# Kernel tuning notes

Measured on AMD Instinct MI355X. Metric: run time of the kernel, lower is better.

## Reference

```python
import jax, jax.numpy as jnp
import numpy as np

BATCH = 8
IMG = 224
PATCH = 16
IN_CH = 8
D_MODEL = 768
DEPTH = 4
D_INNER = 2 * D_MODEL          # 1536
D_STATE = 16
DT_RANK = D_MODEL // 16        # 48
D_CONV = 4
NUM_CLASSES = 1000
EPS = 1e-5


def setup_inputs() -> dict:
    key = jax.random.key(0)
    ks = jax.random.split(key, 16)
    g = lambda i, shape, s=0.02: jax.random.normal(ks[i], shape, jnp.float32) * s
    L = DEPTH
    inp = {}
    inp['x'] = jax.random.normal(ks[0], (BATCH, IN_CH, IMG, IMG), jnp.float32)
    # patch embed: Conv3d(1, D, (1,p,p)) == shared 2D conv applied to every channel
    inp['patch_w'] = g(1, (D_MODEL, PATCH, PATCH))
    inp['patch_b'] = jnp.zeros((D_MODEL,), jnp.float32)
    inp['channel_embed'] = g(2, (IN_CH, D_MODEL))
    # per-block params (stacked over depth)
    inp['norm_w'] = jnp.ones((L, D_MODEL), jnp.float32)
    inp['norm_b'] = jnp.zeros((L, D_MODEL), jnp.float32)
    inp['in_proj_w'] = g(3, (L, 2 * D_INNER, D_MODEL))
    inp['conv_w'] = g(4, (L, D_INNER, D_CONV), 0.1)
    inp['conv_b'] = jnp.zeros((L, D_INNER), jnp.float32)
    inp['x_proj_w'] = g(5, (L, DT_RANK + 2 * D_STATE, D_INNER))
    inp['dt_proj_w'] = g(6, (L, D_INNER, DT_RANK), 0.1)
    inp['dt_proj_b'] = jnp.full((L, D_INNER), -4.6, jnp.float32)  # softplus^-1(0.01)
    inp['A_log'] = jnp.tile(jnp.log(jnp.arange(1, D_STATE + 1, dtype=jnp.float32)), (L, D_INNER, 1))
    inp['D_param'] = jnp.ones((L, D_INNER), jnp.float32)
    inp['ssm_norm_w'] = jnp.ones((L, D_INNER), jnp.float32)
    inp['ssm_norm_b'] = jnp.zeros((L, D_INNER), jnp.float32)
    inp['out_proj_w'] = g(7, (L, D_MODEL, D_INNER), 0.02 / np.sqrt(L))
    # final norm + classification head
    inp['norm_f_w'] = jnp.ones((D_MODEL,), jnp.float32)
    inp['norm_f_b'] = jnp.zeros((D_MODEL,), jnp.float32)
    inp['head_w'] = g(8, (NUM_CLASSES, D_MODEL))
    inp['head_b'] = jnp.zeros((NUM_CLASSES,), jnp.float32)
    return inp


def _ln(x, w, b):
    mu = x.mean(-1, keepdims=True)
    var = ((x - mu) ** 2).mean(-1, keepdims=True)
    return (x - mu) * jax.lax.rsqrt(var + EPS) * w + b


def _silu(x):
    return x * jax.nn.sigmoid(x)


def _mamba(h, ipw, cw, cb, xpw, dtw, dtb, Alog, Dp, snw, snb, opw):
    # h: [B, L, D_MODEL]
    B, Lseq, _ = h.shape
    xz = jnp.einsum('bld,ed->ble', h, ipw)               # [B, L, 2*di]
    x, z = jnp.split(xz, 2, axis=-1)
    # causal depthwise conv1d along L (kernel D_CONV)
    xp = jnp.pad(x, ((0, 0), (D_CONV - 1, 0), (0, 0)))
    xc = cb + sum(xp[:, k:k + Lseq, :] * cw[:, k] for k in range(D_CONV))
    x = _silu(xc)
    dbc = jnp.einsum('bld,ed->ble', x, xpw)              # [B, L, dt_rank+2N]
    dt_r = dbc[..., :DT_RANK]
    Bm = dbc[..., DT_RANK:DT_RANK + D_STATE]
    Cm = dbc[..., DT_RANK + D_STATE:]
    dt = jax.nn.softplus(jnp.einsum('blr,dr->bld', dt_r, dtw) + dtb)  # [B, L, di]
    A = -jnp.exp(Alog)                                    # [di, N]

    def step(hstate, t):
        dt_t, B_t, C_t, x_t = t                           # [B,di],[B,N],[B,N],[B,di]
        dA = jnp.exp(dt_t[..., None] * A)                 # [B, di, N]
        hstate = dA * hstate + (dt_t * x_t)[..., None] * B_t[:, None, :]
        y = jnp.einsum('bdn,bn->bd', hstate, C_t)
        return hstate, y

    h0 = jnp.zeros((B, D_INNER, D_STATE), x.dtype)
    xs = (dt.transpose(1, 0, 2), Bm.transpose(1, 0, 2),
          Cm.transpose(1, 0, 2), x.transpose(1, 0, 2))
    _, ys = jax.lax.scan(step, h0, xs)                    # [L, B, di]
    y = ys.transpose(1, 0, 2) + Dp * x
    y = _ln(y, snw, snb)                                  # norm-after-SSM
    y = y * _silu(z)
    return jnp.einsum('ble,de->bld', y, opw)


def reference(x, patch_w, patch_b, channel_embed, norm_w, norm_b, in_proj_w,
              conv_w, conv_b, x_proj_w, dt_proj_w, dt_proj_b, A_log, D_param,
              ssm_norm_w, ssm_norm_b, out_proj_w, norm_f_w, norm_f_b,
              head_w, head_b):
    B, C, H, W = x.shape
    hg, wg = H // PATCH, W // PATCH
    # shared-filter patch embed per channel: [B,C,hg,wg,D]
    xp = x.reshape(B, C, hg, PATCH, wg, PATCH)
    emb = jnp.einsum('bchpwq,dpq->bchwd', xp, patch_w) + patch_b
    emb = emb + channel_embed[None, :, None, None, :]
    # Channel-First scan order -> token order (h, w, C): [B, hg*wg*C, D]
    tok = emb.transpose(0, 2, 3, 1, 4).reshape(B, hg * wg * C, D_MODEL)

    hidden, residual = tok, None
    for i in range(DEPTH):
        residual = hidden if residual is None else residual + hidden
        hn = _ln(residual, norm_w[i], norm_b[i])
        hidden = _mamba(hn, in_proj_w[i], conv_w[i], conv_b[i], x_proj_w[i],
                        dt_proj_w[i], dt_proj_b[i], A_log[i], D_param[i],
                        ssm_norm_w[i], ssm_norm_b[i], out_proj_w[i])
    residual = residual + hidden
    hf = _ln(residual, norm_f_w, norm_f_b)
    pooled = hf.mean(axis=1)                              # mean pooling head
    return pooled @ head_w.T + head_b
```

## Files before the change

### kernel.cpp

```cpp
#include <hip/hip_runtime.h>
#include <hip/hip_bf16.h>

typedef __hip_bfloat16 bf16;
typedef __attribute__((ext_vector_type(8))) short short8;
typedef __attribute__((ext_vector_type(4))) float float4v;

#define BATCH 8
#define SEQ   1568
#define M_TOK (BATCH*SEQ)
#define DM    768
#define DI    1536
#define DS    16
#define DTR   48
#define NCLS  1000
#define LAYERS 4
#define CHUNK 112
#define NCH   14

__device__ __forceinline__ float b2f(bf16 v){ return __bfloat162float(v); }
__device__ __forceinline__ bf16  f2b(float v){ return __float2bfloat16(v); }
__device__ __forceinline__ float us2f(unsigned short u){
    unsigned v = ((unsigned)u) << 16; float f; __builtin_memcpy(&f, &v, 4); return f;
}
__device__ __forceinline__ void gload_lds16(const void* g, void* l){
    __builtin_amdgcn_global_load_lds(
        (const __attribute__((address_space(1))) void*)g,
        (__attribute__((address_space(3))) void*)l, 16, 0, 0);
}
template<int CTRL>
__device__ __forceinline__ float dpp_add(float p){
    int pi; __builtin_memcpy(&pi, &p, 4);
    int mi = __builtin_amdgcn_update_dpp(pi, pi, CTRL, 0xF, 0xF, false);
    float m; __builtin_memcpy(&m, &mi, 4);
    return p + m;
}

__global__ void detect_dtype(const unsigned short* __restrict__ probe, unsigned* __restrict__ flag)
{
    if (threadIdx.x == 0 && blockIdx.x == 0) flag[0] = (probe[0] == 0) ? 1u : 0u;
}

__global__ __launch_bounds__(256)
void to_bf16(const unsigned* __restrict__ flag, const void* __restrict__ src,
             bf16* __restrict__ dst, int n)
{
    int i = blockIdx.x*256 + threadIdx.x;
    if (i >= n) return;
    dst[i] = flag[0] ? f2b(((const float*)src)[i]) : ((const bf16*)src)[i];
}

__global__ __launch_bounds__(256)
void to_f32(const unsigned* __restrict__ flag, const void* __restrict__ src,
            float* __restrict__ dst, int n)
{
    int i = blockIdx.x*256 + threadIdx.x;
    if (i >= n) return;
    dst[i] = flag[0] ? ((const float*)src)[i] : b2f(((const bf16*)src)[i]);
}

__global__ __launch_bounds__(256)
void gather_patches(const bf16* __restrict__ x, bf16* __restrict__ Ap, int b0)
{
    size_t idx = (size_t)blockIdx.x*256 + threadIdx.x;
    int i = (int)(idx & 255);
    int m = (int)(idx >> 8);
    int b = b0 + m / SEQ, s = m % SEQ;
    int hw = s >> 3, c = s & 7;
    int h = hw / 14, w = hw % 14;
    int p = i >> 4, q = i & 15;
    Ap[idx] = x[(((size_t)(b*8 + c)*224) + h*16 + p)*224 + w*16 + q];
}

__global__ __launch_bounds__(256)
void gemm_mfma(const bf16* __restrict__ A, int lda,
               const bf16* __restrict__ W, int ldw,
               float* __restrict__ Cf, bf16* __restrict__ Cb, int ldc,
               const float* __restrict__ bias, const float* __restrict__ chan,
               int M, int N, int K, int epi)
{
    __shared__ short As[128*40];
    __shared__ short Bs[128*40];
    int tid  = threadIdx.x;
    int m0   = blockIdx.x*128, n0 = blockIdx.y*128;
    int lane = tid & 63, wv = tid >> 6;
    int wm = (wv >> 1)*64, wn = (wv & 1)*64;
    int l15 = lane & 15, quad = lane >> 4;

    float4v acc[4][4];
    #pragma unroll
    for (int i = 0; i < 4; ++i)
        #pragma unroll
        for (int j = 0; j < 4; ++j) acc[i][j] = (float4v){0.f,0.f,0.f,0.f};

    const short8 zv8 = {0,0,0,0,0,0,0,0};
    for (int k0 = 0; k0 < K; k0 += 32) {
        #pragma unroll
        for (int u = 0; u < 2; ++u) {
            int c   = tid*2 + u;
            int row = c >> 2, ch = c & 3;
            bool kok = (k0 + ch*8 + 8) <= K;
            short8 va = (kok && m0 + row < M)
                ? *(const short8*)((const short*)A + (size_t)(m0+row)*lda + k0 + ch*8) : zv8;
            *(short8*)(As + row*40 + ch*8) = va;
            short8 vb = (kok && n0 + row < N)
                ? *(const short8*)((const short*)W + (size_t)(n0+row)*ldw + k0 + ch*8) : zv8;
            *(short8*)(Bs + row*40 + ch*8) = vb;
        }
        __syncthreads();
        short8 av[4], bv[4];
        #pragma unroll
        for (int i = 0; i < 4; ++i) av[i] = *(const short8*)(As + (wm + i*16 + l15)*40 + quad*8);
        #pragma unroll
        for (int j = 0; j < 4; ++j) bv[j] = *(const short8*)(Bs + (wn + j*16 + l15)*40 + quad*8);
        #pragma unroll
        for (int i = 0; i < 4; ++i)
            #pragma unroll
            for (int j = 0; j < 4; ++j)
                acc[i][j] = __builtin_amdgcn_mfma_f32_16x16x32_bf16(av[i], bv[j], acc[i][j], 0, 0, 0);
        __syncthreads();
    }

    #pragma unroll
    for (int i = 0; i < 4; ++i) {
        #pragma unroll
        for (int j = 0; j < 4; ++j) {
            int gn = n0 + wn + j*16 + l15;
            if (gn >= N) continue;
            #pragma unroll
            for (int r = 0; r < 4; ++r) {
                int gm = m0 + wm + i*16 + quad*4 + r;
                if (gm >= M) continue;
                float v = acc[i][j][r];
                size_t off = (size_t)gm*ldc + gn;
                if (epi == 0)      Cb[off] = f2b(v);
                else if (epi == 1) {
                    v += bias[gn];
                    v = (v > 20.f) ? v : log1pf(__expf(v));
                    Cb[off] = f2b(v);
                }
                else if (epi == 2) Cf[off] += v;
                else               Cf[off] = v + bias[gn] + chan[(size_t)(gm & 7)*N + gn];
            }
        }
    }
}

__global__ __launch_bounds__(256)
void gemm_mfma_fast(const bf16* __restrict__ A, int lda,
                    const bf16* __restrict__ W, int ldw,
                    float* __restrict__ Cf, bf16* __restrict__ Cb, int ldc,
                    const float* __restrict__ bias, const float* __restrict__ chan,
                    int N, int K, int epi)
{
    __shared__ short As[128*32];
    __shared__ short Bs[128*32];
    int tid  = threadIdx.x;
    int m0   = blockIdx.x*128, n0 = blockIdx.y*128;
    int lane = tid & 63, wv = tid >> 6;
    int wm = (wv >> 1)*64, wn = (wv & 1)*64;
    int l15 = lane & 15, quad = lane >> 4;

    int srow = (lane >> 2);
    int skof = (lane & 3) * 8;

    float4v acc[4][4];
    #pragma unroll
    for (int i = 0; i < 4; ++i)
        #pragma unroll
        for (int j = 0; j < 4; ++j) acc[i][j] = (float4v){0.f,0.f,0.f,0.f};

    const short* Ab = (const short*)A;
    const short* Wb = (const short*)W;

    for (int k0 = 0; k0 < K; k0 += 32) {
        #pragma unroll
        for (int u = 0; u < 2; ++u) {
            int c = wv*2 + u;
            int row = c*16 + srow;
            gload_lds16(Ab + (size_t)(m0+row)*lda + k0 + skof, As + c*512);
            gload_lds16(Wb + (size_t)(n0+row)*ldw + k0 + skof, Bs + c*512);
        }
        __syncthreads();
        short8 av[4], bv[4];
        #pragma unroll
        for (int i = 0; i < 4; ++i) av[i] = *(const short8*)(As + (wm + i*16 + l15)*32 + quad*8);
        #pragma unroll
        for (int j = 0; j < 4; ++j) bv[j] = *(const short8*)(Bs + (wn + j*16 + l15)*32 + quad*8);
        #pragma unroll
        for (int i = 0; i < 4; ++i)
            #pragma unroll
            for (int j = 0; j < 4; ++j)
                acc[i][j] = __builtin_amdgcn_mfma_f32_16x16x32_bf16(av[i], bv[j], acc[i][j], 0, 0, 0);
        __syncthreads();
    }

    #pragma unroll
    for (int i = 0; i < 4; ++i) {
        #pragma unroll
        for (int j = 0; j < 4; ++j) {
            int gn = n0 + wn + j*16 + l15;
            #pragma unroll
            for (int r = 0; r < 4; ++r) {
                int gm = m0 + wm + i*16 + quad*4 + r;
                float v = acc[i][j][r];
                size_t off = (size_t)gm*ldc + gn;
                if (epi == 0)      Cb[off] = f2b(v);
                else if (epi == 1) {
                    v += bias[gn];
                    v = (v > 20.f) ? v : log1pf(__expf(v));
                    Cb[off] = f2b(v);
                }
                else if (epi == 2) Cf[off] += v;
                else               Cf[off] = v + bias[gn] + chan[(size_t)(gm & 7)*N + gn];
            }
        }
    }
}

__global__ __launch_bounds__(256)
void ln768(const float* __restrict__ X, const float* __restrict__ w,
           const float* __restrict__ bb, bf16* __restrict__ out)
{
    __shared__ float red[8];
    size_t t = blockIdx.x;
    const float* x = X + t*DM;
    float v[3]; float s = 0.f, s2 = 0.f;
    #pragma unroll
    for (int r = 0; r < 3; ++r) {
        v[r] = x[threadIdx.x + 256*r];
        s += v[r]; s2 += v[r]*v[r];
    }
    #pragma unroll
    for (int o = 32; o; o >>= 1) { s += __shfl_down(s, o, 64); s2 += __shfl_down(s2, o, 64); }
    if ((threadIdx.x & 63) == 0) { red[threadIdx.x >> 6] = s; red[(threadIdx.x >> 6) + 4] = s2; }
    __syncthreads();
    s  = red[0]+red[1]+red[2]+red[3];
    s2 = red[4]+red[5]+red[6]+red[7];
    float mu  = s * (1.f/DM);
    float inv = rsqrtf(fmaxf(s2*(1.f/DM) - mu*mu, 0.f) + 1e-5f);
    #pragma unroll
    for (int r = 0; r < 3; ++r) {
        int i = threadIdx.x + 256*r;
        out[t*DM + i] = f2b((v[r]-mu)*inv*w[i] + bb[i]);
    }
}

__global__ __launch_bounds__(256)
void conv_silu(const bf16* __restrict__ xh, const float* __restrict__ cw,
               const float* __restrict__ cb, bf16* __restrict__ xc)
{
    size_t idx = (size_t)blockIdx.x*256 + threadIdx.x;
    int dv = (int)(idx % (DI/8));
    int m  = (int)(idx / (DI/8));
    int b = m / SEQ, t = m % SEQ;
    int d = dv*8;

    float4v cwq[8];
    #pragma unroll
    for (int j = 0; j < 8; ++j) cwq[j] = *(const float4v*)(cw + (size_t)(d+j)*4);

    float acc[8];
    #pragma unroll
    for (int j = 0; j < 8; ++j) acc[j] = cb[d+j];

    #pragma unroll
    for (int k = 0; k < 4; ++k) {
        int tt = t + k - 3;
        if (tt >= 0) {
            short8 v = *(const short8*)((const short*)xh + (size_t)(b*SEQ + tt)*DI + d);
            #pragma unroll
            for (int j = 0; j < 8; ++j)
                acc[j] += us2f((unsigned short)v[j]) * cwq[j][k];
        }
    }
    short8 o;
    #pragma unroll
    for (int j = 0; j < 8; ++j) {
        float sig = 1.f/(1.f + __expf(-acc[j]));
        bf16 r = f2b(acc[j]*sig);
        unsigned short u; __builtin_memcpy(&u, &r, 2); o[j] = (short)u;
    }
    *(short8*)((short*)xc + idx*8) = o;
}


__global__ __launch_bounds__(256)
void scan_pass1(const bf16* __restrict__ dt, const bf16* __restrict__ x,
                const bf16* __restrict__ dbc, const float* __restrict__ Alog,
                float* __restrict__ hend, float* __restrict__ Pprod, int nin2)
{
    __shared__ float dtT[2][64][20], xT[2][64][20];
    __shared__ float BsT[2][16][16];
    int c  = blockIdx.x / nin2;
    int r  = blockIdx.x % nin2;
    int b  = r / 24;
    int d0 = (r % 24) * 64;
    int tid = threadIdx.x;
    int sq = tid & 3;
    int dl = tid >> 2;
    int d  = d0 + dl;

    float4v Aq = *(const float4v*)(Alog + (size_t)d*DS + sq*4);
    float A2[4], h[4];
    #pragma unroll
    for (int k = 0; k < 4; ++k) { A2[k] = -__expf(Aq[k]) * 1.44269504f; h[k] = 0.f; }
    float sdt = 0.f;

    int js = tid >> 4, dg = tid & 15;
    bool doB = tid < 64;
    int j2 = tid >> 2;

    const unsigned short* pdt = (const unsigned short*)dt + ((size_t)b*SEQ + js)*DI + d0 + dg*4;
    const unsigned short* px  = (const unsigned short*)x  + ((size_t)b*SEQ + js)*DI + d0 + dg*4;
    const unsigned short* pbc = (const unsigned short*)dbc + ((size_t)b*SEQ + (j2 & 15))*80 + DTR + sq*4;
    int tbase = c * CHUNK;
    const int NT = CHUNK/16;

    ushort4 vdt, vx, vbc;
    auto stage = [&](int buf){
        dtT[buf][dg*4+0][js] = us2f(vdt.x); dtT[buf][dg*4+1][js] = us2f(vdt.y);
        dtT[buf][dg*4+2][js] = us2f(vdt.z); dtT[buf][dg*4+3][js] = us2f(vdt.w);
        xT [buf][dg*4+0][js] = us2f(vx.x);  xT [buf][dg*4+1][js] = us2f(vx.y);
        xT [buf][dg*4+2][js] = us2f(vx.z);  xT [buf][dg*4+3][js] = us2f(vx.w);
        if (doB)
            *(float4v*)&BsT[buf][j2][sq*4] =
                (float4v){us2f(vbc.x), us2f(vbc.y), us2f(vbc.z), us2f(vbc.w)};
    };
    auto fetch = [&](int T){
        vdt = *(const ushort4*)(pdt + (size_t)(tbase + T*16)*DI);
        vx  = *(const ushort4*)(px  + (size_t)(tbase + T*16)*DI);
        if (doB) vbc = *(const ushort4*)(pbc + (size_t)(tbase + T*16)*80);
    };

    fetch(0); stage(0); fetch(1);
    __syncthreads();

    for (int t = 0; t < NT; ++t) {
        int cur = t & 1;
        if (t+1 < NT) stage(cur^1);
        if (t+2 < NT) fetch(t+2);
        #pragma unroll
        for (int jj = 0; jj < 16; jj += 4) {
            float4v dtq = *(const float4v*)&dtT[cur][dl][jj];
            float4v xq  = *(const float4v*)&xT [cur][dl][jj];
            #pragma unroll
            for (int k2 = 0; k2 < 4; ++k2) {
                float dtv = dtq[k2];
                float dtx = dtv * xq[k2];
                float4v Bq = *(const float4v*)&BsT[cur][jj+k2][sq*4];
                #pragma unroll
                for (int k = 0; k < 4; ++k)
                    h[k] = exp2f(dtv*A2[k])*h[k] + dtx*Bq[k];
                sdt += dtv;
            }
        }
        __syncthreads();
    }
    size_t o = (((size_t)c*nin2 + r)*256 + tid)*4;
    *(float4v*)(hend + o) = (float4v){h[0], h[1], h[2], h[3]};
    *(float4v*)(Pprod + o) = (float4v){exp2f(A2[0]*sdt), exp2f(A2[1]*sdt),
                                       exp2f(A2[2]*sdt), exp2f(A2[3]*sdt)};
}

__global__ __launch_bounds__(256)
void scan_mid(const float* __restrict__ hend, const float* __restrict__ Pprod,
              float* __restrict__ hstart, int nin2)
{
    int r = blockIdx.x, tid = threadIdx.x;
    float4v h = (float4v){0.f,0.f,0.f,0.f};
    *(float4v*)(hstart + ((size_t)r*256 + tid)*4) = h;
    for (int c = 1; c < NCH; ++c) {
        size_t p = (((size_t)(c-1)*nin2 + r)*256 + tid)*4;
        float4v P  = *(const float4v*)(Pprod + p);
        float4v he = *(const float4v*)(hend + p);
        h = P*h + he;
        *(float4v*)(hstart + (((size_t)c*nin2 + r)*256 + tid)*4) = h;
    }
}

__global__ __launch_bounds__(256)
void scan_pass2(const bf16* __restrict__ dt, const bf16* __restrict__ x,
                const bf16* __restrict__ dbc, const float* __restrict__ Alog,
                const float* __restrict__ Dpar, const float* __restrict__ hstart,
                bf16* __restrict__ y, int nin2)
{
    __shared__ float dtT[2][64][20], xT[2][64][20];
    __shared__ float BsT[2][16][16], CsT[2][16][16];
    __shared__ bf16  ys[16][64];
    int c  = blockIdx.x / nin2;
    int r  = blockIdx.x % nin2;
    int b  = r / 24;
    int d0 = (r % 24) * 64;
    int tid = threadIdx.x;
    int sq = tid & 3;
    int dl = tid >> 2;
    int d  = d0 + dl;

    float4v Aq = *(const float4v*)(Alog + (size_t)d*DS + sq*4);
    float A2[4], h[4];
    {
        float4v h0 = *(const float4v*)(hstart + (((size_t)c*nin2 + r)*256 + tid)*4);
        #pragma unroll
        for (int k = 0; k < 4; ++k) { A2[k] = -__expf(Aq[k]) * 1.44269504f; h[k] = h0[k]; }
    }
    float Dv = Dpar[d];

    int js = tid >> 4, dg = tid & 15;
    bool doBC = tid < 128;
    int j2 = (tid & 63) >> 2;

    const unsigned short* pdt = (const unsigned short*)dt + ((size_t)b*SEQ + js)*DI + d0 + dg*4;
    const unsigned short* px  = (const unsigned short*)x  + ((size_t)b*SEQ + js)*DI + d0 + dg*4;
    const unsigned short* pbc = (const unsigned short*)dbc + ((size_t)b*SEQ + j2)*80 + DTR
                                + ((tid >= 64) ? DS : 0) + sq*4;
    float* bc0 = (tid < 64) ? &BsT[0][j2][sq*4] : &CsT[0][j2][sq*4];
    int tbase = c * CHUNK;
    const int NT = CHUNK/16;

    ushort4 vdt, vx, vbc;
    auto stage = [&](int buf){
        dtT[buf][dg*4+0][js] = us2f(vdt.x); dtT[buf][dg*4+1][js] = us2f(vdt.y);
        dtT[buf][dg*4+2][js] = us2f(vdt.z); dtT[buf][dg*4+3][js] = us2f(vdt.w);
        xT [buf][dg*4+0][js] = us2f(vx.x);  xT [buf][dg*4+1][js] = us2f(vx.y);
        xT [buf][dg*4+2][js] = us2f(vx.z);  xT [buf][dg*4+3][js] = us2f(vx.w);
        if (doBC)
            *(float4v*)(bc0 + (size_t)buf*256) =
                (float4v){us2f(vbc.x), us2f(vbc.y), us2f(vbc.z), us2f(vbc.w)};
    };
    auto fetch = [&](int T){
        vdt = *(const ushort4*)(pdt + (size_t)(tbase + T*16)*DI);
        vx  = *(const ushort4*)(px  + (size_t)(tbase + T*16)*DI);
        if (doBC) vbc = *(const ushort4*)(pbc + (size_t)(tbase + T*16)*80);
    };

    fetch(0); stage(0); fetch(1);
    __syncthreads();

    for (int t = 0; t < NT; ++t) {
        int cur = t & 1;
        if (t+1 < NT) stage(cur^1);
        if (t+2 < NT) fetch(t+2);

        #pragma unroll
        for (int jj = 0; jj < 16; jj += 4) {
            float4v dtq = *(const float4v*)&dtT[cur][dl][jj];
            float4v xq  = *(const float4v*)&xT [cur][dl][jj];
            #pragma unroll
            for (int k2 = 0; k2 < 4; ++k2) {
                float dtv = dtq[k2];
                float xv  = xq[k2];
                float dtx = dtv * xv;
                float4v Bq = *(const float4v*)&BsT[cur][jj+k2][sq*4];
                float4v Cq = *(const float4v*)&CsT[cur][jj+k2][sq*4];
                float p = 0.f;
                #pragma unroll
                for (int k = 0; k < 4; ++k) {
                    h[k] = exp2f(dtv*A2[k])*h[k] + dtx*Bq[k];
                    p += h[k]*Cq[k];
                }
                p = dpp_add<0xB1>(p);
                p = dpp_add<0x4E>(p);
                if (sq == 0) ys[jj+k2][dl] = f2b(p + Dv*xv);
            }
        }
        __syncthreads();
        {
            size_t rowm = (size_t)(b*SEQ + tbase + t*16 + js);
            ushort4 vy = *(const ushort4*)((const unsigned short*)&ys[js][0] + dg*4);
            *(ushort4*)((unsigned short*)y + rowm*DI + d0 + dg*4) = vy;
        }
        __syncthreads();
    }
}

__global__ __launch_bounds__(256)
void gate_ln(const bf16* __restrict__ y, const bf16* __restrict__ z,
             const float* __restrict__ w, const float* __restrict__ bb,
             bf16* __restrict__ out)
{
    __shared__ float red[8];
    size_t t = blockIdx.x;
    const bf16* yy = y + t*DI;
    const bf16* zz = z + t*DI;
    float v[6]; float s = 0.f, s2 = 0.f;
    #pragma unroll
    for (int r = 0; r < 6; ++r) {
        v[r] = b2f(yy[threadIdx.x + 256*r]);
        s += v[r]; s2 += v[r]*v[r];
    }
    #pragma unroll
    for (int o = 32; o; o >>= 1) { s += __shfl_down(s, o, 64); s2 += __shfl_down(s2, o, 64); }
    if ((threadIdx.x & 63) == 0) { red[threadIdx.x >> 6] = s; red[(threadIdx.x >> 6) + 4] = s2; }
    __syncthreads();
    s  = red[0]+red[1]+red[2]+red[3];
    s2 = red[4]+red[5]+red[6]+red[7];
    float mu  = s * (1.f/DI);
    float inv = rsqrtf(fmaxf(s2*(1.f/DI) - mu*mu, 0.f) + 1e-5f);
    #pragma unroll
    for (int r = 0; r < 6; ++r) {
        int i = threadIdx.x + 256*r;
        float zv = b2f(zz[i]);
        float sig = 1.f/(1.f + __expf(-zv));
        out[t*DI + i] = f2b(((v[r]-mu)*inv*w[i] + bb[i]) * (zv*sig));
    }
}

__global__ __launch_bounds__(256)
void pool_kernel(const bf16* __restrict__ hf, float* __restrict__ pooled)
{
    int idx = blockIdx.x*256 + threadIdx.x;
    int b = idx / DM, dm = idx % DM;
    const bf16* p = hf + (size_t)b*SEQ*DM + dm;
    float s = 0.f;
    for (int t = 0; t < SEQ; ++t) s += b2f(p[(size_t)t*DM]);
    pooled[idx] = s * (1.f/SEQ);
}

__global__ __launch_bounds__(256)
void head_kernel(const unsigned* __restrict__ flag,
                 const float* __restrict__ pooled, const bf16* __restrict__ hw,
                 const float* __restrict__ hb, void* __restrict__ out)
{
    int idx = blockIdx.x*256 + threadIdx.x;
    if (idx >= BATCH*NCLS) return;
    int b = idx & 7, n = idx >> 3;
    const float* p = pooled + b*DM;
    const unsigned short* w = (const unsigned short*)hw + (size_t)n*DM;
    float acc = hb[n];
    for (int k = 0; k < DM; k += 4) {
        ushort4 wv = *(const ushort4*)(w + k);
        acc += p[k]*us2f(wv.x) + p[k+1]*us2f(wv.y) + p[k+2]*us2f(wv.z) + p[k+3]*us2f(wv.w);
    }
    int o = b*NCLS + n;
    if (flag[0]) ((float*)out)[o] = acc;
    else         ((bf16*)out)[o]  = f2b(acc);
}

extern "C" void kernel_launch(void* const* d_in, const int* in_sizes, int n_in,
                              void* d_out, int out_size, void* d_ws, size_t ws_size,
                              hipStream_t stream)
{
    (void)n_in; (void)out_size;
    dim3 blk(256);

    const bool is_f32[21] = { false, false, true, true, true, true, false, true, true,
                              false, false, true,  true, true, true, true, false,
                              true,  true,  false, true };

    size_t off = 0;
    auto carve = [&](size_t bytes) -> void* {
        void* q = (char*)d_ws + off;
        off += (bytes + 255) & ~(size_t)255;
        return q;
    };

    unsigned* flag = (unsigned*)carve(256);
    void* canon[21];
    for (int i = 0; i < 21; ++i)
        canon[i] = carve((size_t)in_sizes[i] * (is_f32[i] ? 4 : 2));

    float* residual = (float*)carve((size_t)M_TOK*DM*4);
    bf16*  hn       = (bf16*) carve((size_t)M_TOK*DM*2);
    float* pooled   = (float*)carve((size_t)BATCH*DM*4);

    const size_t scanbuf1 = (size_t)NCH*96*256*4;
    const size_t inner1 = 4*(((size_t)SEQ*DI*2 + 255) & ~(size_t)255)
                          + (((size_t)SEQ*80*2 + 255) & ~(size_t)255)
                          + 3*((scanbuf1 + 255) & ~(size_t)255);
    int g = 8;
    while (g > 1 && off + (size_t)g*inner1 > ws_size) g >>= 1;

    bf16* xh  = (bf16*)carve((size_t)g*SEQ*DI*2);
    bf16* zh  = (bf16*)carve((size_t)g*SEQ*DI*2);
    bf16* xc  = (bf16*)carve((size_t)g*SEQ*DI*2);
    bf16* dtb = (bf16*)carve((size_t)g*SEQ*DI*2);
    bf16* dbc = (bf16*)carve((size_t)g*SEQ*80*2);
    float* hend   = (float*)carve((size_t)g*scanbuf1);
    float* Pprod  = (float*)carve((size_t)g*scanbuf1);
    float* hstart = (float*)carve((size_t)g*scanbuf1);
    bf16* Ap    = xh;
    bf16* ybuf  = xh;
    bf16* gated = dtb;

    detect_dtype<<<1, 64, 0, stream>>>((const unsigned short*)d_in[4], flag);
    for (int i = 0; i < 21; ++i) {
        int n = in_sizes[i];
        int gr = (n + 255)/256;
        if (is_f32[i]) to_f32 <<<gr, blk, 0, stream>>>(flag, d_in[i], (float*)canon[i], n);
        else           to_bf16<<<gr, blk, 0, stream>>>(flag, d_in[i], (bf16*) canon[i], n);
    }

    const bf16*  xin   = (const bf16*) canon[0];
    const bf16*  pw    = (const bf16*) canon[1];
    const float* pb    = (const float*)canon[2];
    const float* chan  = (const float*)canon[3];
    const float* nw    = (const float*)canon[4];
    const float* nb    = (const float*)canon[5];
    const bf16*  ipw   = (const bf16*) canon[6];
    const float* cw    = (const float*)canon[7];
    const float* cb    = (const float*)canon[8];
    const bf16*  xpw   = (const bf16*) canon[9];
    const bf16*  dtw   = (const bf16*) canon[10];
    const float* dtbia = (const float*)canon[11];
    const float* Alog  = (const float*)canon[12];
    const float* Dpar  = (const float*)canon[13];
    const float* snw   = (const float*)canon[14];
    const float* snb   = (const float*)canon[15];
    const bf16*  opw   = (const bf16*) canon[16];
    const float* nfw   = (const float*)canon[17];
    const float* nfb   = (const float*)canon[18];
    const bf16*  hw    = (const bf16*) canon[19];
    const float* hb    = (const float*)canon[20];

    const int MG  = g*SEQ;
    const int GXm = (MG + 127)/128;
    const int nin2 = g*24;

    auto launch_gemm = [&](const bf16* A, int lda, const bf16* W, int ldw,
                           float* Cf, bf16* Cb, int ldc,
                           const float* bias, const float* chan_,
                           int M, int N, int K, int epi) {
        dim3 gr((M + 127)/128, (N + 127)/128);
        if ((M & 127) == 0 && (N & 127) == 0 && (K & 31) == 0)
            gemm_mfma_fast<<<gr, blk, 0, stream>>>(A, lda, W, ldw, Cf, Cb, ldc,
                                                   bias, chan_, N, K, epi);
        else
            gemm_mfma<<<gr, blk, 0, stream>>>(A, lda, W, ldw, Cf, Cb, ldc,
                                              bias, chan_, M, N, K, epi);
    };

    for (int b0 = 0; b0 < BATCH; b0 += g) {
        gather_patches<<<MG, blk, 0, stream>>>(xin, Ap, b0);
        launch_gemm(Ap, 256, pw, 256,
                    residual + (size_t)b0*SEQ*DM, nullptr, DM,
                    pb, chan, MG, DM, 256, 3);
    }

    for (int l = 0; l < LAYERS; ++l) {
        ln768<<<M_TOK, blk, 0, stream>>>(residual, nw + l*DM, nb + l*DM, hn);
        for (int b0 = 0; b0 < BATCH; b0 += g) {
            const bf16* hng = hn + (size_t)b0*SEQ*DM;
            launch_gemm(hng, DM, ipw + (size_t)l*2*DI*DM, DM,
                        nullptr, xh, DI, nullptr, nullptr, MG, DI, DM, 0);
            launch_gemm(hng, DM, ipw + (size_t)l*2*DI*DM + (size_t)DI*DM, DM,
                        nullptr, zh, DI, nullptr, nullptr, MG, DI, DM, 0);
            conv_silu<<<(MG*(DI/8))/256, blk, 0, stream>>>(xh, cw + (size_t)l*DI*4, cb + l*DI, xc);
            launch_gemm(xc, DI, xpw + (size_t)l*80*DI, DI,
                        nullptr, dbc, 80, nullptr, nullptr, MG, 80, DI, 0);
            launch_gemm(dbc, 80, dtw + (size_t)l*DI*DTR, DTR,
                        nullptr, dtb, DI, dtbia + l*DI, nullptr, MG, DI, DTR, 1);
            scan_pass1<<<(NCH-1)*nin2, blk, 0, stream>>>(dtb, xc, dbc,
                                                         Alog + (size_t)l*DI*DS,
                                                         hend, Pprod, nin2);
            scan_mid<<<nin2, blk, 0, stream>>>(hend, Pprod, hstart, nin2);
            scan_pass2<<<NCH*nin2, blk, 0, stream>>>(dtb, xc, dbc,
                                                     Alog + (size_t)l*DI*DS,
                                                     Dpar + l*DI, hstart, ybuf, nin2);
            gate_ln<<<MG, blk, 0, stream>>>(ybuf, zh, snw + l*DI, snb + l*DI, gated);
            launch_gemm(gated, DI, opw + (size_t)l*DM*DI, DI,
                        residual + (size_t)b0*SEQ*DM, nullptr, DM,
                        nullptr, nullptr, MG, DM, DI, 2);
        }
    }

    ln768<<<M_TOK, blk, 0, stream>>>(residual, nfw, nfb, hn);
    pool_kernel<<<(BATCH*DM)/256, blk, 0, stream>>>(hn, pooled);
    head_kernel<<<(BATCH*NCLS + 255)/256, blk, 0, stream>>>(flag, pooled, hw, hb, d_out);
}
```

Baseline: 3.515 ms.

## Pad x_proj/dt_proj GEMMs for fast path, vectorize gate_ln, split pooling

The x_proj and dt_proj weights are zero-padded (80 to 128 rows, 48 to 64 columns) so both small GEMMs meet the aligned-shape condition and use the fast MFMA kernel. The dbc buffer stride becomes 128 and the scan kernels read it at that stride. gate_ln now uses 192 threads that each handle 8 contiguous bf16 values with vector loads and stores. Mean pooling is split into a per-chunk partial-sum kernel and a small finish kernel, giving more parallelism than the old kernel where each thread summed 1568 rows. Padding adds wasted FLOPs and extra per-call weight-padding kernels.

```diff
diff --git a/kernel.cpp b/kernel.cpp
--- a/kernel.cpp
+++ b/kernel.cpp
@@ -16,6 +16,7 @@
 #define LAYERS 4
 #define CHUNK 112
 #define NCH   14
+#define DBCW  128
 
 __device__ __forceinline__ float b2f(bf16 v){ return __bfloat162float(v); }
 __device__ __forceinline__ bf16  f2b(float v){ return __float2bfloat16(v); }
@@ -56,6 +57,27 @@
     int i = blockIdx.x*256 + threadIdx.x;
     if (i >= n) return;
     dst[i] = flag[0] ? ((const float*)src)[i] : b2f(((const bf16*)src)[i]);
+}
+
+__global__ __launch_bounds__(256)
+void pad_xpw(const bf16* __restrict__ src, bf16* __restrict__ dst)
+{
+    int idx = blockIdx.x*256 + threadIdx.x;
+    if (idx >= LAYERS*128*DI) return;
+    int l = idx / (128*DI);
+    int r = (idx / DI) % 128;
+    int c = idx % DI;
+    dst[idx] = (r < 80) ? src[((size_t)l*80 + r)*DI + c] : f2b(0.f);
+}
+__global__ __launch_bounds__(256)
+void pad_dtw(const bf16* __restrict__ src, bf16* __restrict__ dst)
+{
+    int idx = blockIdx.x*256 + threadIdx.x;
+    if (idx >= LAYERS*DI*64) return;
+    int l = idx / (DI*64);
+    int d = (idx / 64) % DI;
+    int c = idx % 64;
+    dst[idx] = (c < DTR) ? src[((size_t)l*DI + d)*DTR + c] : f2b(0.f);
 }
 
 __global__ __launch_bounds__(256)
@@ -312,7 +334,7 @@
 
     const unsigned short* pdt = (const unsigned short*)dt + ((size_t)b*SEQ + js)*DI + d0 + dg*4;
     const unsigned short* px  = (const unsigned short*)x  + ((size_t)b*SEQ + js)*DI + d0 + dg*4;
-    const unsigned short* pbc = (const unsigned short*)dbc + ((size_t)b*SEQ + (j2 & 15))*80 + DTR + sq*4;
+    const unsigned short* pbc = (const unsigned short*)dbc + ((size_t)b*SEQ + (j2 & 15))*DBCW + DTR + sq*4;
     int tbase = c * CHUNK;
     const int NT = CHUNK/16;
 
@@ -329,7 +351,7 @@
     auto fetch = [&](int T){
         vdt = *(const ushort4*)(pdt + (size_t)(tbase + T*16)*DI);
         vx  = *(const ushort4*)(px  + (size_t)(tbase + T*16)*DI);
-        if (doB) vbc = *(const ushort4*)(pbc + (size_t)(tbase + T*16)*80);
+        if (doB) vbc = *(const ushort4*)(pbc + (size_t)(tbase + T*16)*DBCW);
     };
 
     fetch(0); stage(0); fetch(1);
@@ -411,7 +433,7 @@
 
     const unsigned short* pdt = (const unsigned short*)dt + ((size_t)b*SEQ + js)*DI + d0 + dg*4;
     const unsigned short* px  = (const unsigned short*)x  + ((size_t)b*SEQ + js)*DI + d0 + dg*4;
-    const unsigned short* pbc = (const unsigned short*)dbc + ((size_t)b*SEQ + j2)*80 + DTR
+    const unsigned short* pbc = (const unsigned short*)dbc + ((size_t)b*SEQ + j2)*DBCW + DTR
                                 + ((tid >= 64) ? DS : 0) + sq*4;
     float* bc0 = (tid < 64) ? &BsT[0][j2][sq*4] : &CsT[0][j2][sq*4];
     int tbase = c * CHUNK;
@@ -430,7 +452,7 @@
     auto fetch = [&](int T){
         vdt = *(const ushort4*)(pdt + (size_t)(tbase + T*16)*DI);
         vx  = *(const ushort4*)(px  + (size_t)(tbase + T*16)*DI);
-        if (doBC) vbc = *(const ushort4*)(pbc + (size_t)(tbase + T*16)*80);
+        if (doBC) vbc = *(const ushort4*)(pbc + (size_t)(tbase + T*16)*DBCW);
     };
 
     fetch(0); stage(0); fetch(1);
@@ -473,46 +495,74 @@
     }
 }
 
-__global__ __launch_bounds__(256)
+__global__ __launch_bounds__(192)
 void gate_ln(const bf16* __restrict__ y, const bf16* __restrict__ z,
              const float* __restrict__ w, const float* __restrict__ bb,
              bf16* __restrict__ out)
 {
-    __shared__ float red[8];
+    __shared__ float red[6];
     size_t t = blockIdx.x;
-    const bf16* yy = y + t*DI;
-    const bf16* zz = z + t*DI;
-    float v[6]; float s = 0.f, s2 = 0.f;
-    #pragma unroll
-    for (int r = 0; r < 6; ++r) {
-        v[r] = b2f(yy[threadIdx.x + 256*r]);
-        s += v[r]; s2 += v[r]*v[r];
+    int tid = threadIdx.x;
+    int i0 = tid*8;
+    short8 y8 = *(const short8*)((const short*)y + t*DI + i0);
+    short8 z8 = *(const short8*)((const short*)z + t*DI + i0);
+    float vy[8];
+    float s = 0.f, s2 = 0.f;
+    #pragma unroll
+    for (int j = 0; j < 8; ++j) {
+        vy[j] = us2f((unsigned short)y8[j]);
+        s += vy[j]; s2 += vy[j]*vy[j];
     }
     #pragma unroll
     for (int o = 32; o; o >>= 1) { s += __shfl_down(s, o, 64); s2 += __shfl_down(s2, o, 64); }
-    if ((threadIdx.x & 63) == 0) { red[threadIdx.x >> 6] = s; red[(threadIdx.x >> 6) + 4] = s2; }
+    if ((tid & 63) == 0) { red[tid >> 6] = s; red[(tid >> 6) + 3] = s2; }
     __syncthreads();
-    s  = red[0]+red[1]+red[2]+red[3];
-    s2 = red[4]+red[5]+red[6]+red[7];
+    s  = red[0]+red[1]+red[2];
+    s2 = red[3]+red[4]+red[5];
     float mu  = s * (1.f/DI);
     float inv = rsqrtf(fmaxf(s2*(1.f/DI) - mu*mu, 0.f) + 1e-5f);
-    #pragma unroll
-    for (int r = 0; r < 6; ++r) {
-        int i = threadIdx.x + 256*r;
-        float zv = b2f(zz[i]);
+    float4v w0 = *(const float4v*)(w + i0);
+    float4v w1 = *(const float4v*)(w + i0 + 4);
+    float4v b0 = *(const float4v*)(bb + i0);
+    float4v b1 = *(const float4v*)(bb + i0 + 4);
+    short8 o8;
+    #pragma unroll
+    for (int j = 0; j < 8; ++j) {
+        float zv = us2f((unsigned short)z8[j]);
         float sig = 1.f/(1.f + __expf(-zv));
-        out[t*DI + i] = f2b(((v[r]-mu)*inv*w[i] + bb[i]) * (zv*sig));
-    }
-}
-
-__global__ __launch_bounds__(256)
-void pool_kernel(const bf16* __restrict__ hf, float* __restrict__ pooled)
+        float wj = (j < 4) ? w0[j] : w1[j-4];
+        float bj = (j < 4) ? b0[j] : b1[j-4];
+        bf16 rr = f2b(((vy[j]-mu)*inv*wj + bj) * (zv*sig));
+        unsigned short u; __builtin_memcpy(&u, &rr, 2); o8[j] = (short)u;
+    }
+    *(short8*)((short*)out + t*DI + i0) = o8;
+}
+
+__global__ __launch_bounds__(256)
+void pool_partial(const bf16* __restrict__ hf, float* __restrict__ part)
+{
+    int blk = blockIdx.x;
+    int b = blk / NCH, c = blk % NCH;
+    int tid = threadIdx.x;
+    const bf16* p = hf + ((size_t)b*SEQ + c*CHUNK)*DM;
+    float s0 = 0.f, s1 = 0.f, s2 = 0.f;
+    for (int t = 0; t < CHUNK; ++t) {
+        s0 += b2f(p[(size_t)t*DM + tid]);
+        s1 += b2f(p[(size_t)t*DM + tid + 256]);
+        s2 += b2f(p[(size_t)t*DM + tid + 512]);
+    }
+    part[(size_t)blk*DM + tid]       = s0;
+    part[(size_t)blk*DM + tid + 256] = s1;
+    part[(size_t)blk*DM + tid + 512] = s2;
+}
+
+__global__ __launch_bounds__(256)
+void pool_finish(const float* __restrict__ part, float* __restrict__ pooled)
 {
     int idx = blockIdx.x*256 + threadIdx.x;
     int b = idx / DM, dm = idx % DM;
-    const bf16* p = hf + (size_t)b*SEQ*DM + dm;
     float s = 0.f;
-    for (int t = 0; t < SEQ; ++t) s += b2f(p[(size_t)t*DM]);
+    for (int c = 0; c < NCH; ++c) s += part[((size_t)b*NCH + c)*DM + dm];
     pooled[idx] = s * (1.f/SEQ);
 }
 
@@ -562,10 +612,13 @@
     float* residual = (float*)carve((size_t)M_TOK*DM*4);
     bf16*  hn       = (bf16*) carve((size_t)M_TOK*DM*2);
     float* pooled   = (float*)carve((size_t)BATCH*DM*4);
+    float* poolpart = (float*)carve((size_t)BATCH*NCH*DM*4);
+    bf16*  xpw_pad  = (bf16*) carve((size_t)LAYERS*128*DI*2);
+    bf16*  dtw_pad  = (bf16*) carve((size_t)LAYERS*DI*64*2);
 
     const size_t scanbuf1 = (size_t)NCH*96*256*4;
     const size_t inner1 = 4*(((size_t)SEQ*DI*2 + 255) & ~(size_t)255)
-                          + (((size_t)SEQ*80*2 + 255) & ~(size_t)255)
+                          + (((size_t)SEQ*DBCW*2 + 255) & ~(size_t)255)
                           + 3*((scanbuf1 + 255) & ~(size_t)255);
     int g = 8;
     while (g > 1 && off + (size_t)g*inner1 > ws_size) g >>= 1;
@@ -574,7 +627,7 @@
     bf16* zh  = (bf16*)carve((size_t)g*SEQ*DI*2);
     bf16* xc  = (bf16*)carve((size_t)g*SEQ*DI*2);
     bf16* dtb = (bf16*)carve((size_t)g*SEQ*DI*2);
-    bf16* dbc = (bf16*)carve((size_t)g*SEQ*80*2);
+    bf16* dbc = (bf16*)carve((size_t)g*SEQ*DBCW*2);
     float* hend   = (float*)carve((size_t)g*scanbuf1);
     float* Pprod  = (float*)carve((size_t)g*scanbuf1);
     float* hstart = (float*)carve((size_t)g*scanbuf1);
@@ -612,6 +665,9 @@
     const bf16*  hw    = (const bf16*) canon[19];
     const float* hb    = (const float*)canon[20];
 
+    pad_xpw<<<(LAYERS*128*DI + 255)/256, blk, 0, stream>>>(xpw, xpw_pad);
+    pad_dtw<<<(LAYERS*DI*64 + 255)/256, blk, 0, stream>>>(dtw, dtw_pad);
+
     const int MG  = g*SEQ;
     const int GXm = (MG + 127)/128;
     const int nin2 = g*24;
@@ -645,10 +701,10 @@
             launch_gemm(hng, DM, ipw + (size_t)l*2*DI*DM + (size_t)DI*DM, DM,
                         nullptr, zh, DI, nullptr, nullptr, MG, DI, DM, 0);
             conv_silu<<<(MG*(DI/8))/256, blk, 0, stream>>>(xh, cw + (size_t)l*DI*4, cb + l*DI, xc);
-            launch_gemm(xc, DI, xpw + (size_t)l*80*DI, DI,
-                        nullptr, dbc, 80, nullptr, nullptr, MG, 80, DI, 0);
-            launch_gemm(dbc, 80, dtw + (size_t)l*DI*DTR, DTR,
-                        nullptr, dtb, DI, dtbia + l*DI, nullptr, MG, DI, DTR, 1);
+            launch_gemm(xc, DI, xpw_pad + (size_t)l*128*DI, DI,
+                        nullptr, dbc, DBCW, nullptr, nullptr, MG, 128, DI, 0);
+            launch_gemm(dbc, DBCW, dtw_pad + (size_t)l*DI*64, 64,
+                        nullptr, dtb, DI, dtbia + l*DI, nullptr, MG, DI, 64, 1);
             scan_pass1<<<(NCH-1)*nin2, blk, 0, stream>>>(dtb, xc, dbc,
                                                          Alog + (size_t)l*DI*DS,
                                                          hend, Pprod, nin2);
@@ -656,7 +712,7 @@
             scan_pass2<<<NCH*nin2, blk, 0, stream>>>(dtb, xc, dbc,
                                                      Alog + (size_t)l*DI*DS,
                                                      Dpar + l*DI, hstart, ybuf, nin2);
-            gate_ln<<<MG, blk, 0, stream>>>(ybuf, zh, snw + l*DI, snb + l*DI, gated);
+            gate_ln<<<MG, dim3(192), 0, stream>>>(ybuf, zh, snw + l*DI, snb + l*DI, gated);
             launch_gemm(gated, DI, opw + (size_t)l*DM*DI, DI,
                         residual + (size_t)b0*SEQ*DM, nullptr, DM,
                         nullptr, nullptr, MG, DM, DI, 2);
@@ -664,6 +720,7 @@
     }
 
     ln768<<<M_TOK, blk, 0, stream>>>(residual, nfw, nfb, hn);
-    pool_kernel<<<(BATCH*DM)/256, blk, 0, stream>>>(hn, pooled);
+    pool_partial<<<BATCH*NCH, blk, 0, stream>>>(hn, poolpart);
+    pool_finish<<<(BATCH*DM)/256, blk, 0, stream>>>(poolpart, pooled);
     head_kernel<<<(BATCH*NCLS + 255)/256, blk, 0, stream>>>(flag, pooled, hw, hb, d_out);
 }
```

Result: slower. 3.755 ms (+6.8%).
